# Performance work log

Hardware: AMD Instinct MI355X
Metric: run time of the kernel (lower is better)

Reference implementation:

```python
import jax, jax.numpy as jnp
import numpy as np

NUM_EMBEDDING = 8192
EMBEDDING_DIM = 512
BS = 16384
NEG_SLOPE = 0.01  # torch LeakyReLU default


def setup_inputs() -> dict:
    key = jax.random.key(0)
    k1, k2, k3, k4, k5, k6, k7 = jax.random.split(key, 7)
    d, K = EMBEDDING_DIM, NUM_EMBEDDING
    s1 = 1.0 / np.sqrt(d)
    return {
        "encoded_eeg": jax.random.normal(k1, (BS, d), dtype=jnp.float32),
        "encoded_mel": jax.random.normal(k2, (BS, d), dtype=jnp.float32),
        "embeddings": jax.random.normal(k3, (K, d), dtype=jnp.float32),
        "W1": jax.random.uniform(k4, (d, d), jnp.float32, -s1, s1),
        "b1": jax.random.uniform(k5, (d,), jnp.float32, -s1, s1),
        "W2": jax.random.uniform(k6, (K, d), jnp.float32, -s1, s1),
        "b2": jax.random.uniform(k7, (K,), jnp.float32, -s1, s1),
    }


def reference(encoded_eeg, encoded_mel, embeddings, W1, b1, W2, b2):
    # --- nearest-codebook indices for mel (detached in original) ---
    flat_mel = encoded_mel.reshape(-1, EMBEDDING_DIM)
    dists = (jnp.sum(embeddings ** 2, axis=1)[None, :]
             + jnp.sum(flat_mel ** 2, axis=1, keepdims=True)
             - 2.0 * flat_mel @ embeddings.T)  # [BS, K]
    mel_indices = jnp.argmin(dists, axis=-1)  # [BS]

    # --- small MLP logits over eeg ---
    flat_eeg = encoded_eeg.reshape(-1, EMBEDDING_DIM)
    h = flat_eeg @ W1.T + b1
    h = jnp.where(h >= 0, h, NEG_SLOPE * h)  # LeakyReLU
    logits = h @ W2.T + b2  # [BS, K]

    eeg_indices = jnp.argmax(logits, axis=-1)
    acc_rate = jnp.mean((eeg_indices == mel_indices).astype(jnp.float32))

    # cross entropy (mean over batch)
    logp = jax.nn.log_softmax(logits, axis=-1)
    loss = -jnp.mean(jnp.take_along_axis(logp, mel_indices[:, None], axis=1))
    return (loss, acc_rate)
```

## Files before the change

### kernel.cpp

```cpp
#include <hip/hip_runtime.h>
#include <hip/hip_bf16.h>
#include <hip/hip_fp8.h>

#define BSZ 16384
#define DIM 512
#define NEMB 8192
#define NEG 0.01f
#define NSPLIT 8
#define NG 128

typedef __attribute__((ext_vector_type(8))) short short8;
typedef __attribute__((ext_vector_type(4))) float f32x4;
typedef __attribute__((ext_vector_type(2))) long long2v;
typedef __attribute__((ext_vector_type(4))) int i32x4;
typedef __attribute__((ext_vector_type(8))) int i32x8;

typedef const __attribute__((address_space(1))) void GVT;
typedef __attribute__((address_space(3))) void LVT;

__device__ __forceinline__ void gl_lds16(const void* g, void* l) {
    __builtin_amdgcn_global_load_lds((GVT*)g, (LVT*)l, 16, 0, 0);
}

__device__ __forceinline__ float bf2f(unsigned short u) {
    union { unsigned int i; float f; } c; c.i = ((unsigned int)u) << 16; return c.f;
}
__device__ __forceinline__ unsigned short f2bf(float f) {
    union { __hip_bfloat16 h; unsigned short u; } c; c.h = __float2bfloat16(f); return c.u;
}
__device__ __forceinline__ unsigned char f2fp8(float f) {
    __hip_fp8_e4m3 t(f); return (unsigned char)t.__x;
}
__device__ __forceinline__ unsigned int fkey(float f) {
    unsigned int u = __float_as_uint(f);
    return u ^ ((unsigned int)((int)u >> 31) | 0x80000000u);
}

__device__ __forceinline__ size_t pack_addr(int r, int k) {
    int kg = k >> 6, ko = k & 63;
    int half = ko >> 5, lq = (ko & 31) >> 3, sub = ko & 7;
    int L = lq * 16 + (r & 15);
    return ((size_t)((r >> 4) * 8 + kg) << 10) + (size_t)(L << 4) + (half << 3) + sub;
}

__device__ __forceinline__ void pipe_barrier6() {
    asm volatile("s_waitcnt vmcnt(6) lgkmcnt(0)\ns_barrier" ::: "memory");
}
__device__ __forceinline__ void plain_barrier() {
    asm volatile("s_barrier" ::: "memory");
}

#define ISSUE6(G, BUF) do { \
    int Gm = (G) & (NG - 1); \
    size_t aoff = (size_t)((Gm & 7) << 10); \
    size_t boff = aoff + ((size_t)(Gm >> 3) << 15); \
    gl_lds16(gA8 + aoff,         &sA8[BUF][uWd]); \
    gl_lds16(gA8 + aoff + 32768, &sA8[BUF][uWd + 4096]); \
    gl_lds16(gB8 + boff,         &sB8[BUF][uWd]); \
} while (0)

#define COMPUTE8(BA, BB) do { \
    i32x8 fa[2], fb[4]; \
    _Pragma("unroll") for (int i = 0; i < 2; i++) { \
        i32x4 al = *(const i32x4*)&sA8[BA][offA[i]]; \
        i32x4 ah = *(const i32x4*)&sA8[BB][offA[i]]; \
        fa[i] = __builtin_shufflevector(al, ah, 0, 1, 2, 3, 4, 5, 6, 7); \
    } \
    _Pragma("unroll") for (int i = 0; i < 4; i++) { \
        i32x4 bl = *(const i32x4*)&sB8[BA][offB[i]]; \
        i32x4 bh = *(const i32x4*)&sB8[BB][offB[i]]; \
        fb[i] = __builtin_shufflevector(bl, bh, 0, 1, 2, 3, 4, 5, 6, 7); \
    } \
    __builtin_amdgcn_s_setprio(1); \
    _Pragma("unroll") for (int mi = 0; mi < 2; mi++) \
        _Pragma("unroll") for (int ni = 0; ni < 4; ni++) \
            acc[mi][ni] = __builtin_amdgcn_mfma_scale_f32_16x16x128_f8f6f4( \
                fa[mi], fb[ni], acc[mi][ni], 0, 0, 0, 0x7F7F7F7Fu, 0, 0x7F7F7F7Fu); \
    __builtin_amdgcn_s_setprio(0); \
} while (0)

__global__ void k_prep(const float* __restrict__ eeg, const float* __restrict__ mel,
                       const float* __restrict__ emb, const float* __restrict__ W2,
                       const float* __restrict__ W1,
                       unsigned short* __restrict__ o_eeg, unsigned short* __restrict__ o_w1,
                       unsigned char* __restrict__ o_mel8, unsigned char* __restrict__ o_emb8,
                       unsigned char* __restrict__ o_w28,
                       float* __restrict__ enorm,
                       float* __restrict__ acc2, int* __restrict__ cnt) {
    int bid = blockIdx.x, tid = threadIdx.x;
    if (bid == 0 && tid == 0) { acc2[0] = 0.f; acc2[1] = 0.f; *cnt = 0; }
    if (bid < 1024) {
        const int n_big = BSZ * DIM / 4;
        const int n_mid = NEMB * DIM / 4;
        const int n_w1  = DIM * DIM / 4;
        const int total = n_big * 2 + n_mid * 2 + n_w1;
        for (int i = bid * 256 + tid; i < total; i += 1024 * 256) {
            int j = i;
            if (j < n_big) {
                float4 v = ((const float4*)eeg)[j];
                ushort4 o; o.x = f2bf(v.x); o.y = f2bf(v.y); o.z = f2bf(v.z); o.w = f2bf(v.w);
                ((ushort4*)o_eeg)[j] = o;
            } else if ((j -= n_big) < n_w1) {
                float4 v = ((const float4*)W1)[j];
                ushort4 o; o.x = f2bf(v.x); o.y = f2bf(v.y); o.z = f2bf(v.z); o.w = f2bf(v.w);
                ((ushort4*)o_w1)[j] = o;
            } else if ((j -= n_w1) < n_big) {
                float4 v = ((const float4*)mel)[j];
                uchar4 o; o.x = f2fp8(v.x); o.y = f2fp8(v.y); o.z = f2fp8(v.z); o.w = f2fp8(v.w);
                *(uchar4*)(o_mel8 + pack_addr(j >> 7, (j & 127) * 4)) = o;
            } else if ((j -= n_big) < n_mid) {
                float4 v = ((const float4*)emb)[j];
                uchar4 o; o.x = f2fp8(v.x); o.y = f2fp8(v.y); o.z = f2fp8(v.z); o.w = f2fp8(v.w);
                *(uchar4*)(o_emb8 + pack_addr(j >> 7, (j & 127) * 4)) = o;
            } else {
                j -= n_mid;
                float4 v = ((const float4*)W2)[j];
                uchar4 o; o.x = f2fp8(v.x); o.y = f2fp8(v.y); o.z = f2fp8(v.z); o.w = f2fp8(v.w);
                *(uchar4*)(o_w28 + pack_addr(j >> 7, (j & 127) * 4)) = o;
            }
        }
    } else {
        int w = tid >> 6, lane = tid & 63;
        int row0 = (bid - 1024) * 8 + w * 2;
        #pragma unroll
        for (int t = 0; t < 2; t++) {
            int row = row0 + t;
            const float4* p = (const float4*)(emb + (size_t)row * DIM) + lane * 2;
            float4 a = p[0], b = p[1];
            float s = a.x*a.x + a.y*a.y + a.z*a.z + a.w*a.w
                    + b.x*b.x + b.y*b.y + b.z*b.z + b.w*b.w;
            #pragma unroll
            for (int d = 1; d < 64; d <<= 1) s += __shfl_xor(s, d);
            if (lane == 0) enorm[row] = s;
        }
    }
}

__launch_bounds__(256, 2)
__global__ void k_hgemm(const unsigned short* __restrict__ A,
                        const unsigned short* __restrict__ B,
                        const float* __restrict__ b1,
                        unsigned short* __restrict__ H,
                        unsigned char* __restrict__ H8) {
    __shared__ __align__(16) unsigned short sA[4096], sB[4096];
    int tid = threadIdx.x;
    int w = tid >> 6, lane = tid & 63;
    int wr = w >> 1, wc = w & 1;
    int lquad = lane >> 4, l15 = lane & 15;
    int mt = blockIdx.x >> 2, nt = blockIdx.x & 3;
    int m0 = mt * 128, n0 = nt * 128;

    int e0 = w * 512 + lane * 8;
    int r0 = e0 >> 5, ce = e0 & 31;
    const unsigned short* gA0 = A + (m0 + r0) * DIM + ce;
    const unsigned short* gA1 = gA0 + 64 * DIM;
    const unsigned short* gB0 = B + (n0 + r0) * DIM + ce;
    const unsigned short* gB1 = gB0 + 64 * DIM;
    unsigned short* lA0 = sA + w * 512;  unsigned short* lA1 = sA + (w + 4) * 512;
    unsigned short* lB0 = sB + w * 512;  unsigned short* lB1 = sB + (w + 4) * 512;

    int offA[4], offB[4];
    #pragma unroll
    for (int i = 0; i < 4; i++) {
        offA[i] = (wr * 64 + i * 16 + l15) * 32 + lquad * 8;
        offB[i] = (wc * 64 + i * 16 + l15) * 32 + lquad * 8;
    }

    f32x4 acc[4][4];
    #pragma unroll
    for (int mi = 0; mi < 4; mi++)
        #pragma unroll
        for (int ni = 0; ni < 4; ni++) acc[mi][ni] = 0;

    for (int kk = 0; kk < 16; kk++) {
        gl_lds16(gA0, lA0); gl_lds16(gA1, lA1);
        gl_lds16(gB0, lB0); gl_lds16(gB1, lB1);
        gA0 += 32; gA1 += 32; gB0 += 32; gB1 += 32;
        __syncthreads();
        short8 af[4], bf_[4];
        #pragma unroll
        for (int i = 0; i < 4; i++) {
            af[i]  = *(const short8*)&sA[offA[i]];
            bf_[i] = *(const short8*)&sB[offB[i]];
        }
        #pragma unroll
        for (int mi = 0; mi < 4; mi++)
            #pragma unroll
            for (int ni = 0; ni < 4; ni++)
                acc[mi][ni] = __builtin_amdgcn_mfma_f32_16x16x32_bf16(af[mi], bf_[ni], acc[mi][ni], 0, 0, 0);
        __syncthreads();
    }

    #pragma unroll
    for (int ni = 0; ni < 4; ni++) {
        int col = n0 + wc * 64 + ni * 16 + l15;
        float bv = b1[col];
        #pragma unroll
        for (int mi = 0; mi < 4; mi++) {
            int rowb = m0 + wr * 64 + mi * 16 + lquad * 4;
            #pragma unroll
            for (int rg = 0; rg < 4; rg++) {
                float v = acc[mi][ni][rg] + bv;
                v = v >= 0.f ? v : NEG * v;
                H[(rowb + rg) * DIM + col] = f2bf(v);
                H8[pack_addr(rowb + rg, col)] = f2fp8(v);
            }
        }
    }
}

__launch_bounds__(256, 3)
__global__ void k_big(const unsigned char* __restrict__ Mel8,
                      const unsigned char* __restrict__ Emb8,
                      const unsigned char* __restrict__ H8,
                      const unsigned char* __restrict__ W28,
                      const float* __restrict__ enorm,
                      const float* __restrict__ b2,
                      float* __restrict__ p_s,
                      unsigned int* __restrict__ p_pmax,
                      unsigned int* __restrict__ p_pmin) {
    __shared__ __align__(16) unsigned char sA8[4][8192], sB8[4][4096];
    __shared__ float sAux[1024];
    int tid = threadIdx.x;
    int w = tid >> 6, lane = tid & 63;
    int lquad = lane >> 4, l15 = lane & 15;
    int bid = blockIdx.x;
    int is_logits = bid & 1;
    int id = bid >> 1;
    int mt = id >> 3, split = id & 7;
    int m0 = mt * 128, nbase = split * (NEMB / NSPLIT);

    int uWd = w * 1024;
    const unsigned char* gA8 = (is_logits ? H8 : Mel8) + (size_t)(m0 + 16 * w) * 512 + lane * 16;
    const unsigned char* gB8 = (is_logits ? W28 : Emb8) + (size_t)(nbase + 16 * w) * 512 + lane * 16;

    int offA[2], offB[4];
    #pragma unroll
    for (int i = 0; i < 2; i++) offA[i] = (w * 2 + i) * 1024 + lane * 16;
    #pragma unroll
    for (int i = 0; i < 4; i++) offB[i] = i * 1024 + lane * 16;

    #pragma unroll
    for (int j = 0; j < 4; j++) {
        int c = tid + j * 256;
        sAux[c] = is_logits ? b2[nbase + c] : (enorm[nbase + c] - 512.0f);
    }

    ISSUE6(0, 0);
    ISSUE6(1, 1);
    ISSUE6(2, 2);
    ISSUE6(3, 3);

    f32x4 acc[2][4];
    #pragma unroll
    for (int mi = 0; mi < 2; mi++)
        #pragma unroll
        for (int ni = 0; ni < 4; ni++) acc[mi][ni] = 0;

    float s[8];
    unsigned int pbest[8];
    unsigned int pinit = is_logits ? 0u : 0xFFFFFFFFu;
    #pragma unroll
    for (int r = 0; r < 8; r++) { s[r] = 0.f; pbest[r] = pinit; }

    for (int g = 0; g < NG; g += 2) {
        int sa = g & 3, sb = sa + 1;
        pipe_barrier6();
        COMPUTE8(sa, sb);
        plain_barrier();
        ISSUE6(g + 4, sa);
        ISSUE6(g + 5, sb);
        if (((g + 1) & 7) == 7) {
            int c0off = ((g + 1) >> 3) << 6;
            if (is_logits) {
                #pragma unroll
                for (int ni = 0; ni < 4; ni++) {
                    int j = c0off + ni * 16 + l15;
                    float bb = sAux[j];
                    unsigned int ic = (unsigned int)(NEMB - 1 - (nbase + j));
                    #pragma unroll
                    for (int mi = 0; mi < 2; mi++)
                        #pragma unroll
                        for (int rg = 0; rg < 4; rg++) {
                            float logit = acc[mi][ni][rg] + bb;
                            int r = mi * 4 + rg;
                            s[r] += __expf(logit);
                            unsigned int pk = (fkey(logit) & 0xFFFFE000u) | ic;
                            pbest[r] = pbest[r] > pk ? pbest[r] : pk;
                            acc[mi][ni][rg] = 0.f;
                        }
                }
            } else {
                #pragma unroll
                for (int ni = 0; ni < 4; ni++) {
                    int j = c0off + ni * 16 + l15;
                    float en = sAux[j];
                    unsigned int cl = (unsigned int)(nbase + j);
                    #pragma unroll
                    for (int mi = 0; mi < 2; mi++)
                        #pragma unroll
                        for (int rg = 0; rg < 4; rg++) {
                            float d = fmaf(-2.f, acc[mi][ni][rg], en);
                            unsigned int pk = (fkey(d) & 0xFFFFE000u) | cl;
                            int r = mi * 4 + rg;
                            pbest[r] = pbest[r] < pk ? pbest[r] : pk;
                            acc[mi][ni][rg] = 0.f;
                        }
                }
            }
        }
    }

    if (is_logits) {
        #pragma unroll
        for (int r = 0; r < 8; r++)
            #pragma unroll
            for (int d = 1; d < 16; d <<= 1) {
                s[r] += __shfl_xor(s[r], d);
                unsigned int o = (unsigned int)__shfl_xor((int)pbest[r], d);
                pbest[r] = pbest[r] > o ? pbest[r] : o;
            }
        if (l15 == 0) {
            #pragma unroll
            for (int mi = 0; mi < 2; mi++)
                #pragma unroll
                for (int rg = 0; rg < 4; rg++) {
                    int row = w * 32 + mi * 16 + lquad * 4 + rg;
                    int pidx = split * BSZ + m0 + row;
                    p_s[pidx] = s[mi * 4 + rg];
                    p_pmax[pidx] = pbest[mi * 4 + rg];
                }
        }
    } else {
        #pragma unroll
        for (int r = 0; r < 8; r++)
            #pragma unroll
            for (int d = 1; d < 16; d <<= 1) {
                unsigned int o = (unsigned int)__shfl_xor((int)pbest[r], d);
                pbest[r] = pbest[r] < o ? pbest[r] : o;
            }
        if (l15 == 0) {
            #pragma unroll
            for (int mi = 0; mi < 2; mi++)
                #pragma unroll
                for (int rg = 0; rg < 4; rg++) {
                    int row = w * 32 + mi * 16 + lquad * 4 + rg;
                    p_pmin[split * BSZ + m0 + row] = pbest[mi * 4 + rg];
                }
        }
    }
}

__global__ void k_tail(const float* __restrict__ p_s, const unsigned int* __restrict__ p_pmax,
                       const unsigned int* __restrict__ p_pmin,
                       const unsigned short* __restrict__ H,
                       const float* __restrict__ W2,
                       const float* __restrict__ b2,
                       float* __restrict__ acc2, int* __restrict__ cnt,
                       float* __restrict__ out) {
    __shared__ int s_idx[256];
    __shared__ float s_l1[256], s_match[256];
    __shared__ float s_d[4];
    int bid = blockIdx.x, tid = threadIdx.x;
    int w = tid >> 6, lane = tid & 63;
    int r = bid * 256 + tid;

    float S = 0.f; unsigned int PM = 0u, PN = 0xFFFFFFFFu;
    #pragma unroll
    for (int sp = 0; sp < NSPLIT; sp++) {
        S += p_s[sp * BSZ + r];
        unsigned int a = p_pmax[sp * BSZ + r];
        PM = PM > a ? PM : a;
        unsigned int b = p_pmin[sp * BSZ + r];
        PN = PN < b ? PN : b;
    }
    int eidx = (NEMB - 1) - (int)(PM & 0x1FFFu);
    int midx = (int)(PN & 0x1FFFu);
    s_idx[tid] = midx;
    s_l1[tid] = __logf(S) - b2[midx];
    s_match[tid] = (eidx == midx) ? 1.f : 0.f;
    __syncthreads();

    float d0 = 0.f, d1 = 0.f;
    for (int j = 0; j < 64; j++) {
        int rr = w * 64 + j;
        int ridx = s_idx[rr];
        uint4 hv = *(const uint4*)(H + (size_t)(bid * 256 + rr) * DIM + lane * 8);
        const float4* wp = (const float4*)(W2 + (size_t)ridx * DIM + lane * 8);
        float4 w0 = wp[0], w1 = wp[1];
        float p = bf2f((unsigned short)(hv.x & 0xffff)) * w0.x + bf2f((unsigned short)(hv.x >> 16)) * w0.y
                + bf2f((unsigned short)(hv.y & 0xffff)) * w0.z + bf2f((unsigned short)(hv.y >> 16)) * w0.w
                + bf2f((unsigned short)(hv.z & 0xffff)) * w1.x + bf2f((unsigned short)(hv.z >> 16)) * w1.y
                + bf2f((unsigned short)(hv.w & 0xffff)) * w1.z + bf2f((unsigned short)(hv.w >> 16)) * w1.w;
        if (j & 1) d1 += p; else d0 += p;
    }
    float ds = d0 + d1;
    #pragma unroll
    for (int d = 1; d < 64; d <<= 1) ds += __shfl_xor(ds, d);
    if (lane == 0) s_d[w] = ds;

    __syncthreads();
    for (int st = 128; st > 0; st >>= 1) {
        if (tid < st) { s_l1[tid] += s_l1[tid + st]; s_match[tid] += s_match[tid + st]; }
        __syncthreads();
    }
    if (tid == 0) {
        float loss_blk = s_l1[0] - (s_d[0] + s_d[1] + s_d[2] + s_d[3]);
        atomicAdd(&acc2[0], loss_blk * (1.0f / BSZ));
        atomicAdd(&acc2[1], s_match[0] * (1.0f / BSZ));
        __threadfence();
        if (atomicAdd(cnt, 1) == 63) {
            float L = atomicAdd(&acc2[0], 0.f);
            float M = atomicAdd(&acc2[1], 0.f);
            out[0] = L; out[1] = M;
        }
    }
}

extern "C" void kernel_launch(void* const* d_in, const int* in_sizes, int n_in,
                              void* d_out, int out_size, void* d_ws, size_t ws_size,
                              hipStream_t stream) {
    const float* eeg = (const float*)d_in[0];
    const float* mel = (const float*)d_in[1];
    const float* emb = (const float*)d_in[2];
    const float* W1  = (const float*)d_in[3];
    const float* b1  = (const float*)d_in[4];
    const float* W2  = (const float*)d_in[5];
    const float* b2  = (const float*)d_in[6];
    float* out = (float*)d_out;

    unsigned short* ws_eeg = (unsigned short*)d_ws;
    unsigned short* ws_w1  = ws_eeg + (size_t)BSZ * DIM;
    unsigned short* ws_h   = ws_w1  + (size_t)DIM * DIM;
    unsigned char*  ws_h8  = (unsigned char*)(ws_h + (size_t)BSZ * DIM);
    unsigned char*  ws_mel8 = ws_h8  + (size_t)BSZ * DIM;
    unsigned char*  ws_emb8 = ws_mel8 + (size_t)BSZ * DIM;
    unsigned char*  ws_w28  = ws_emb8 + (size_t)NEMB * DIM;
    float* ws_en  = (float*)(ws_w28 + (size_t)NEMB * DIM);
    float* p_s    = ws_en + NEMB;
    unsigned int* p_pmax = (unsigned int*)(p_s + (size_t)NSPLIT * BSZ);
    unsigned int* p_pmin = p_pmax + (size_t)NSPLIT * BSZ;
    float* acc2   = (float*)(p_pmin + (size_t)NSPLIT * BSZ);
    int*   cnt    = (int*)(acc2 + 2);

    k_prep<<<2048, 256, 0, stream>>>(eeg, mel, emb, W2, W1,
                                     ws_eeg, ws_w1, ws_mel8, ws_emb8, ws_w28,
                                     ws_en, acc2, cnt);
    k_hgemm<<<(BSZ / 128) * (DIM / 128), 256, 0, stream>>>(ws_eeg, ws_w1, b1, ws_h, ws_h8);
    k_big<<<(BSZ / 128) * NSPLIT * 2, 256, 0, stream>>>(ws_mel8, ws_emb8, ws_h8, ws_w28,
                                                        ws_en, b2, p_s, p_pmax, p_pmin);
    k_tail<<<BSZ / 256, 256, 0, stream>>>(p_s, p_pmax, p_pmin, ws_h, W2, b2, acc2, cnt, out);
}
```

Measured before the change: 382.4 us.

## Keep A-operand fragments in registers and stream only B tiles through LDS

Each block's 128-row A tile (K=512 in fp8) is now loaded once from global memory into registers at kernel start, instead of being re-streamed into LDS for every 64-column N chunk. The main loop streams only the B operand through a 4-stage LDS ring, issuing one async load per step, and the wait count drops to match. This removes most LDS traffic and global re-reads of A and halves the shared-memory footprint, which could allow more resident blocks. In exchange it costs 64 extra VGPRs per thread for the A fragments, adding register pressure under the launch bound of 3 blocks per CU.

After: 352.9 us. -7.7%, faster.

```diff
diff --git a/kernel.cpp b/kernel.cpp
--- a/kernel.cpp
+++ b/kernel.cpp
@@ -43,40 +43,69 @@
     return ((size_t)((r >> 4) * 8 + kg) << 10) + (size_t)(L << 4) + (half << 3) + sub;
 }
 
-__device__ __forceinline__ void pipe_barrier6() {
-    asm volatile("s_waitcnt vmcnt(6) lgkmcnt(0)\ns_barrier" ::: "memory");
+__device__ __forceinline__ void pipe_barrier2() {
+    asm volatile("s_waitcnt vmcnt(2) lgkmcnt(0)\ns_barrier" ::: "memory");
 }
 __device__ __forceinline__ void plain_barrier() {
     asm volatile("s_barrier" ::: "memory");
 }
-
-#define ISSUE6(G, BUF) do { \
+__device__ __forceinline__ void drain_vm() {
+    asm volatile("s_waitcnt vmcnt(0)" ::: "memory");
+}
+
+#define ISSUE_B(G, BUF) do { \
     int Gm = (G) & (NG - 1); \
-    size_t aoff = (size_t)((Gm & 7) << 10); \
-    size_t boff = aoff + ((size_t)(Gm >> 3) << 15); \
-    gl_lds16(gA8 + aoff,         &sA8[BUF][uWd]); \
-    gl_lds16(gA8 + aoff + 32768, &sA8[BUF][uWd + 4096]); \
-    gl_lds16(gB8 + boff,         &sB8[BUF][uWd]); \
+    size_t boff = ((size_t)(Gm >> 3) << 15) + (size_t)((Gm & 7) << 10); \
+    gl_lds16(gB8 + boff, &sB8[BUF][uWd]); \
 } while (0)
 
-#define COMPUTE8(BA, BB) do { \
-    i32x8 fa[2], fb[4]; \
-    _Pragma("unroll") for (int i = 0; i < 2; i++) { \
-        i32x4 al = *(const i32x4*)&sA8[BA][offA[i]]; \
-        i32x4 ah = *(const i32x4*)&sA8[BB][offA[i]]; \
-        fa[i] = __builtin_shufflevector(al, ah, 0, 1, 2, 3, 4, 5, 6, 7); \
-    } \
+#define COMPUTE8(KP, SA, SB) do { \
+    i32x8 fb[4]; \
     _Pragma("unroll") for (int i = 0; i < 4; i++) { \
-        i32x4 bl = *(const i32x4*)&sB8[BA][offB[i]]; \
-        i32x4 bh = *(const i32x4*)&sB8[BB][offB[i]]; \
+        i32x4 bl = *(const i32x4*)&sB8[SA][offB[i]]; \
+        i32x4 bh = *(const i32x4*)&sB8[SB][offB[i]]; \
         fb[i] = __builtin_shufflevector(bl, bh, 0, 1, 2, 3, 4, 5, 6, 7); \
     } \
     __builtin_amdgcn_s_setprio(1); \
     _Pragma("unroll") for (int mi = 0; mi < 2; mi++) \
         _Pragma("unroll") for (int ni = 0; ni < 4; ni++) \
             acc[mi][ni] = __builtin_amdgcn_mfma_scale_f32_16x16x128_f8f6f4( \
-                fa[mi], fb[ni], acc[mi][ni], 0, 0, 0, 0x7F7F7F7Fu, 0, 0x7F7F7F7Fu); \
+                fa8[mi][KP], fb[ni], acc[mi][ni], 0, 0, 0, 0x7F7F7F7Fu, 0, 0x7F7F7F7Fu); \
     __builtin_amdgcn_s_setprio(0); \
+} while (0)
+
+#define EPILOGUE(NT) do { \
+    int c0off = (NT) << 6; \
+    if (is_logits) { \
+        _Pragma("unroll") for (int ni = 0; ni < 4; ni++) { \
+            int j = c0off + ni * 16 + l15; \
+            float bb = sAux[j]; \
+            unsigned int ic = (unsigned int)(NEMB - 1 - (nbase + j)); \
+            _Pragma("unroll") for (int mi = 0; mi < 2; mi++) \
+                _Pragma("unroll") for (int rg = 0; rg < 4; rg++) { \
+                    float logit = acc[mi][ni][rg] + bb; \
+                    int r = mi * 4 + rg; \
+                    s[r] += __expf(logit); \
+                    unsigned int pk = (fkey(logit) & 0xFFFFE000u) | ic; \
+                    pbest[r] = pbest[r] > pk ? pbest[r] : pk; \
+                    acc[mi][ni][rg] = 0.f; \
+                } \
+        } \
+    } else { \
+        _Pragma("unroll") for (int ni = 0; ni < 4; ni++) { \
+            int j = c0off + ni * 16 + l15; \
+            float en = sAux[j]; \
+            unsigned int cl = (unsigned int)(nbase + j); \
+            _Pragma("unroll") for (int mi = 0; mi < 2; mi++) \
+                _Pragma("unroll") for (int rg = 0; rg < 4; rg++) { \
+                    float d = fmaf(-2.f, acc[mi][ni][rg], en); \
+                    unsigned int pk = (fkey(d) & 0xFFFFE000u) | cl; \
+                    int r = mi * 4 + rg; \
+                    pbest[r] = pbest[r] < pk ? pbest[r] : pk; \
+                    acc[mi][ni][rg] = 0.f; \
+                } \
+        } \
+    } \
 } while (0)
 
 __global__ void k_prep(const float* __restrict__ eeg, const float* __restrict__ mel,
@@ -219,7 +248,7 @@
                       float* __restrict__ p_s,
                       unsigned int* __restrict__ p_pmax,
                       unsigned int* __restrict__ p_pmin) {
-    __shared__ __align__(16) unsigned char sA8[4][8192], sB8[4][4096];
+    __shared__ __align__(16) unsigned char sB8[4][4096];
     __shared__ float sAux[1024];
     int tid = threadIdx.x;
     int w = tid >> 6, lane = tid & 63;
@@ -231,12 +260,10 @@
     int m0 = mt * 128, nbase = split * (NEMB / NSPLIT);
 
     int uWd = w * 1024;
-    const unsigned char* gA8 = (is_logits ? H8 : Mel8) + (size_t)(m0 + 16 * w) * 512 + lane * 16;
+    const unsigned char* gAb = (is_logits ? H8 : Mel8);
     const unsigned char* gB8 = (is_logits ? W28 : Emb8) + (size_t)(nbase + 16 * w) * 512 + lane * 16;
 
-    int offA[2], offB[4];
-    #pragma unroll
-    for (int i = 0; i < 2; i++) offA[i] = (w * 2 + i) * 1024 + lane * 16;
+    int offB[4];
     #pragma unroll
     for (int i = 0; i < 4; i++) offB[i] = i * 1024 + lane * 16;
 
@@ -246,10 +273,23 @@
         sAux[c] = is_logits ? b2[nbase + c] : (enorm[nbase + c] - 512.0f);
     }
 
-    ISSUE6(0, 0);
-    ISSUE6(1, 1);
-    ISSUE6(2, 2);
-    ISSUE6(3, 3);
+    i32x8 fa8[2][4];
+    #pragma unroll
+    for (int mi = 0; mi < 2; mi++)
+        #pragma unroll
+        for (int kp = 0; kp < 4; kp++) {
+            const unsigned char* p = gAb
+                + ((size_t)(((m0 >> 4) + 2 * w + mi) * 8 + 2 * kp) << 10) + lane * 16;
+            i32x4 lo = *(const i32x4*)p;
+            i32x4 hi = *(const i32x4*)(p + 1024);
+            fa8[mi][kp] = __builtin_shufflevector(lo, hi, 0, 1, 2, 3, 4, 5, 6, 7);
+        }
+    drain_vm();
+
+    ISSUE_B(0, 0);
+    ISSUE_B(1, 1);
+    ISSUE_B(2, 2);
+    ISSUE_B(3, 3);
 
     f32x4 acc[2][4];
     #pragma unroll
@@ -263,52 +303,12 @@
     #pragma unroll
     for (int r = 0; r < 8; r++) { s[r] = 0.f; pbest[r] = pinit; }
 
-    for (int g = 0; g < NG; g += 2) {
-        int sa = g & 3, sb = sa + 1;
-        pipe_barrier6();
-        COMPUTE8(sa, sb);
-        plain_barrier();
-        ISSUE6(g + 4, sa);
-        ISSUE6(g + 5, sb);
-        if (((g + 1) & 7) == 7) {
-            int c0off = ((g + 1) >> 3) << 6;
-            if (is_logits) {
-                #pragma unroll
-                for (int ni = 0; ni < 4; ni++) {
-                    int j = c0off + ni * 16 + l15;
-                    float bb = sAux[j];
-                    unsigned int ic = (unsigned int)(NEMB - 1 - (nbase + j));
-                    #pragma unroll
-                    for (int mi = 0; mi < 2; mi++)
-                        #pragma unroll
-                        for (int rg = 0; rg < 4; rg++) {
-                            float logit = acc[mi][ni][rg] + bb;
-                            int r = mi * 4 + rg;
-                            s[r] += __expf(logit);
-                            unsigned int pk = (fkey(logit) & 0xFFFFE000u) | ic;
-                            pbest[r] = pbest[r] > pk ? pbest[r] : pk;
-                            acc[mi][ni][rg] = 0.f;
-                        }
-                }
-            } else {
-                #pragma unroll
-                for (int ni = 0; ni < 4; ni++) {
-                    int j = c0off + ni * 16 + l15;
-                    float en = sAux[j];
-                    unsigned int cl = (unsigned int)(nbase + j);
-                    #pragma unroll
-                    for (int mi = 0; mi < 2; mi++)
-                        #pragma unroll
-                        for (int rg = 0; rg < 4; rg++) {
-                            float d = fmaf(-2.f, acc[mi][ni][rg], en);
-                            unsigned int pk = (fkey(d) & 0xFFFFE000u) | cl;
-                            int r = mi * 4 + rg;
-                            pbest[r] = pbest[r] < pk ? pbest[r] : pk;
-                            acc[mi][ni][rg] = 0.f;
-                        }
-                }
-            }
-        }
+    for (int gg = 0; gg < NG; gg += 8) {
+        pipe_barrier2(); COMPUTE8(0, 0, 1); plain_barrier(); ISSUE_B(gg + 4, 0); ISSUE_B(gg + 5, 1);
+        pipe_barrier2(); COMPUTE8(1, 2, 3); plain_barrier(); ISSUE_B(gg + 6, 2); ISSUE_B(gg + 7, 3);
+        pipe_barrier2(); COMPUTE8(2, 0, 1); plain_barrier(); ISSUE_B(gg + 8, 0); ISSUE_B(gg + 9, 1);
+        pipe_barrier2(); COMPUTE8(3, 2, 3); plain_barrier(); ISSUE_B(gg + 10, 2); ISSUE_B(gg + 11, 3);
+        EPILOGUE(gg >> 3);
     }
 
     if (is_logits) {
```
